# Optimization experiments

Measured on AMD Instinct MI355X. Metric: run time of the kernel, lower is better.

## Reference

```python
import jax, jax.numpy as jnp
import numpy as np

SHIFT_MAX = 20.0  # max |offset| in pixels; padded margin is (M-N)/2 = 32

def setup_inputs() -> dict:
    key = jax.random.key(0)
    k1, k2 = jax.random.split(key)
    B, M, N, C = 2048, 128, 64, 4
    padded_obj = jax.random.normal(k1, (B, M, M, 1), dtype=jnp.float32)
    # channel-format offsets (B,1,2,C): [...,0,:] = x (col) shift, [...,1,:] = y (row) shift
    positions = (jax.random.uniform(k2, (B, 1, 2, C), dtype=jnp.float32) - 0.5) * 2.0 * SHIFT_MAX
    return {"padded_obj": padded_obj, "positions": positions, "N": N}


def _bilinear_extract(padded_obj, positions, N):
    # padded_obj: (B,M,M,1), positions: (B,1,2,C) -> patches (B,N,N,C)
    # Equivalent to: translate each (per-channel) copy of the object by -offset
    # with bilinear interpolation and zero fill, then crop the central NxN.
    B, M = padded_obj.shape[0], padded_obj.shape[1]
    C = positions.shape[-1]
    img = padded_obj[..., 0]                       # (B,M,M)
    ox = positions[:, 0, 0, :]                     # (B,C) x (column) offset
    oy = positions[:, 0, 1, :]                     # (B,C) y (row) offset
    c0 = (M - N) // 2                              # crop origin
    r = jnp.arange(N, dtype=positions.dtype)
    # sample coordinates in source image: out(r,c) = img(r + c0 + oy, c + c0 + ox)
    yy = r[None, None, :] + c0 + oy[..., None]     # (B,C,N)
    xx = r[None, None, :] + c0 + ox[..., None]     # (B,C,N)
    y0 = jnp.floor(yy)
    x0 = jnp.floor(xx)
    wy = (yy - y0)[:, :, :, None]                  # (B,C,N,1) row frac
    wx = (xx - x0)[:, :, None, :]                  # (B,C,1,N) col frac
    y0i = y0.astype(jnp.int32)
    x0i = x0.astype(jnp.int32)
    b_idx = jnp.arange(B)[:, None, None, None]

    def gather(yi, xi):
        # yi: (B,C,N) rows, xi: (B,C,N) cols -> (B,C,N,N) with zero fill OOB
        valid = ((yi[:, :, :, None] >= 0) & (yi[:, :, :, None] < M)
                 & (xi[:, :, None, :] >= 0) & (xi[:, :, None, :] < M))
        yc = jnp.clip(yi, 0, M - 1)[:, :, :, None]
        xc = jnp.clip(xi, 0, M - 1)[:, :, None, :]
        vals = img[b_idx, yc, xc]                  # (B,C,N,N)
        return jnp.where(valid, vals, jnp.zeros((), vals.dtype))

    v00 = gather(y0i, x0i)
    v01 = gather(y0i, x0i + 1)
    v10 = gather(y0i + 1, x0i)
    v11 = gather(y0i + 1, x0i + 1)
    patch = (v00 * (1 - wy) * (1 - wx) + v01 * (1 - wy) * wx
             + v10 * wy * (1 - wx) + v11 * wy * wx)   # (B,C,N,N)
    return jnp.transpose(patch, (0, 2, 3, 1))          # (B,N,N,C)


def reference(padded_obj, positions, N):
    return _bilinear_extract(padded_obj, positions, N)
```

## Files before the change

kernel.cpp:

```cpp
#include <hip/hip_runtime.h>


constexpr int Mdim   = 128;
constexpr int Npatch = 64;
constexpr int Cc     = 4;
constexpr int C0     = 32;
constexpr int SROWS  = 74;

__global__ __launch_bounds__(512, 8) void extract_patches_kernel(
    const float* __restrict__ img,
    const float* __restrict__ pos,
    float* __restrict__ out)
{
    __shared__ float lds[SROWS * Mdim];

    const int bid  = blockIdx.x;
    const int b    = bid >> 1;
    const int h    = bid & 1;
    const float* __restrict__ imgb = img + (size_t)b * (Mdim * Mdim);
    const float* __restrict__ pb   = pos + (size_t)b * (2 * Cc);

    const int tid  = threadIdx.x;
    const int lane = tid & 63;
    const int wave = tid >> 6;

    float w00[Cc], w01[Cc], w10[Cc], w11[Cc];
    int   iyv[Cc], ixv[Cc];
#pragma unroll
    for (int c = 0; c < Cc; ++c) {
        const float ox = pb[c];
        const float oy = pb[Cc + c];
        const float fx = floorf(ox);
        const float fy = floorf(oy);
        const float wx = ox - fx;
        const float wy = oy - fy;
        ixv[c] = C0 + (int)fx;
        iyv[c] = C0 + (int)fy;
        w00[c] = (1.0f - wy) * (1.0f - wx);
        w01[c] = (1.0f - wy) * wx;
        w10[c] = wy * (1.0f - wx);
        w11[c] = wy * wx;
    }

    int min_iy = min(min(iyv[0], iyv[1]), min(iyv[2], iyv[3]));
    int r0 = min(min_iy + 32 * h, Mdim - SROWS);

    const float* src = imgb + r0 * Mdim;
    for (int w = wave; w < (SROWS * Mdim) / 256; w += 8) {
        const float* g = src + w * 256 + lane * 4;
        __builtin_amdgcn_global_load_lds(
            (const __attribute__((address_space(1))) void*)g,
            (__attribute__((address_space(3))) void*)&lds[w * 256],
            16, 0, 0);
    }

    __syncthreads();

    const int j   = tid & 63;
    const int s   = tid >> 6;
    const int li0 = s * 4;

    int   a[Cc];
    float p0[Cc], p1[Cc];
#pragma unroll
    for (int c = 0; c < Cc; ++c) {
        a[c] = (iyv[c] + 32 * h + li0 - r0) * Mdim + ixv[c] + j;
        p0[c] = lds[a[c]];
        p1[c] = lds[a[c] + 1];
    }

    float* obase = out + (((size_t)b * Npatch + 32 * h + li0) * Npatch + j) * Cc;
#pragma unroll
    for (int k = 0; k < 4; ++k) {
        float4 o;
        float* res = reinterpret_cast<float*>(&o);
#pragma unroll
        for (int c = 0; c < Cc; ++c) {
            a[c] += Mdim;
            const float n0 = lds[a[c]];
            const float n1 = lds[a[c] + 1];
            res[c] = w00[c] * p0[c] + w01[c] * p1[c] + w10[c] * n0 + w11[c] * n1;
            p0[c] = n0;
            p1[c] = n1;
        }
        *reinterpret_cast<float4*>(obase + (size_t)k * Npatch * Cc) = o;
    }
}

extern "C" void kernel_launch(void* const* d_in, const int* in_sizes, int n_in,
                              void* d_out, int out_size, void* d_ws, size_t ws_size,
                              hipStream_t stream) {
    const float* img = (const float*)d_in[0];
    const float* pos = (const float*)d_in[1];
    float* out = (float*)d_out;

    const int B = in_sizes[0] / (Mdim * Mdim);
    extract_patches_kernel<<<dim3(2 * B), dim3(512), 0, stream>>>(img, pos, out);
}
```

Baseline: 231.8 us.

## Make blocks persistent over eight work items with double-buffered LDS prefetch

Each block now processes eight (batch, half) items instead of one, and double-buffers the LDS staging so the global-to-LDS copy of the next item overlaps the interpolation of the current one, controlled by explicit vmcnt waits and barriers. The goal is to hide load latency and amortize block launch and setup costs. In exchange LDS per block doubles, occupancy drops to 4 blocks, and the grid shrinks to 512 blocks, which may underfill the GPU. The staging window grows to 76 rows so the 5 chunks per wave come out even.

After: 235.7 us. Within noise of the previous version (+1.7%).

```diff
diff --git a/kernel.cpp b/kernel.cpp
--- a/kernel.cpp
+++ b/kernel.cpp
@@ -5,85 +5,125 @@
 constexpr int Npatch = 64;
 constexpr int Cc     = 4;
 constexpr int C0     = 32;
-constexpr int SROWS  = 74;
+constexpr int SROWS  = 76;
+constexpr int CHUNKS = (SROWS * Mdim) / 256;
+constexpr int CPW    = 5;
+constexpr int ITEMS  = 8;
 
-__global__ __launch_bounds__(512, 8) void extract_patches_kernel(
+__global__ __launch_bounds__(512, 4) void extract_patches_kernel(
     const float* __restrict__ img,
     const float* __restrict__ pos,
     float* __restrict__ out)
 {
-    __shared__ float lds[SROWS * Mdim];
-
-    const int bid  = blockIdx.x;
-    const int b    = bid >> 1;
-    const int h    = bid & 1;
-    const float* __restrict__ imgb = img + (size_t)b * (Mdim * Mdim);
-    const float* __restrict__ pb   = pos + (size_t)b * (2 * Cc);
+    __shared__ float lds[2][SROWS * Mdim];
 
     const int tid  = threadIdx.x;
     const int lane = tid & 63;
     const int wave = tid >> 6;
 
-    float w00[Cc], w01[Cc], w10[Cc], w11[Cc];
-    int   iyv[Cc], ixv[Cc];
+    const int item0 = blockIdx.x * ITEMS;
+    const int b0    = item0 >> 1;
+
+    float oxv[4][Cc], oyv[4][Cc];
 #pragma unroll
-    for (int c = 0; c < Cc; ++c) {
-        const float ox = pb[c];
-        const float oy = pb[Cc + c];
-        const float fx = floorf(ox);
-        const float fy = floorf(oy);
-        const float wx = ox - fx;
-        const float wy = oy - fy;
-        ixv[c] = C0 + (int)fx;
-        iyv[c] = C0 + (int)fy;
-        w00[c] = (1.0f - wy) * (1.0f - wx);
-        w01[c] = (1.0f - wy) * wx;
-        w10[c] = wy * (1.0f - wx);
-        w11[c] = wy * wx;
+    for (int q = 0; q < 4; ++q) {
+        const float* pb = pos + (size_t)(b0 + q) * (2 * Cc);
+#pragma unroll
+        for (int c = 0; c < Cc; ++c) { oxv[q][c] = pb[c]; oyv[q][c] = pb[Cc + c]; }
     }
 
-    int min_iy = min(min(iyv[0], iyv[1]), min(iyv[2], iyv[3]));
-    int r0 = min(min_iy + 32 * h, Mdim - SROWS);
+    int   iyC[Cc], ixC[Cc], r0C; float wC[Cc][4];
+    int   iyN[Cc], ixN[Cc], r0N; float wN[Cc][4];
 
-    const float* src = imgb + r0 * Mdim;
-    for (int w = wave; w < (SROWS * Mdim) / 256; w += 8) {
-        const float* g = src + w * 256 + lane * 4;
-        __builtin_amdgcn_global_load_lds(
-            (const __attribute__((address_space(1))) void*)g,
-            (__attribute__((address_space(3))) void*)&lds[w * 256],
-            16, 0, 0);
-    }
-
-    __syncthreads();
-
-    const int j   = tid & 63;
-    const int s   = tid >> 6;
-    const int li0 = s * 4;
-
-    int   a[Cc];
-    float p0[Cc], p1[Cc];
-#pragma unroll
-    for (int c = 0; c < Cc; ++c) {
-        a[c] = (iyv[c] + 32 * h + li0 - r0) * Mdim + ixv[c] + j;
-        p0[c] = lds[a[c]];
-        p1[c] = lds[a[c] + 1];
-    }
-
-    float* obase = out + (((size_t)b * Npatch + 32 * h + li0) * Npatch + j) * Cc;
-#pragma unroll
-    for (int k = 0; k < 4; ++k) {
-        float4 o;
-        float* res = reinterpret_cast<float*>(&o);
+    auto make_consts = [&](int t, int* iy, int* ix, float (*w)[4], int& r0) {
+        const int q = (t >> 1) & 3, h = t & 1;
+        int mn = Mdim;
 #pragma unroll
         for (int c = 0; c < Cc; ++c) {
-            a[c] += Mdim;
-            const float n0 = lds[a[c]];
-            const float n1 = lds[a[c] + 1];
-            res[c] = w00[c] * p0[c] + w01[c] * p1[c] + w10[c] * n0 + w11[c] * n1;
-            p0[c] = n0;
-            p1[c] = n1;
+            const float ox = oxv[q][c], oy = oyv[q][c];
+            const float fx = floorf(ox), fy = floorf(oy);
+            const float wx = ox - fx,   wy = oy - fy;
+            ix[c] = C0 + (int)fx;
+            iy[c] = C0 + (int)fy;
+            w[c][0] = (1.f - wy) * (1.f - wx);
+            w[c][1] = (1.f - wy) * wx;
+            w[c][2] = wy * (1.f - wx);
+            w[c][3] = wy * wx;
+            mn = min(mn, iy[c]);
         }
-        *reinterpret_cast<float4*>(obase + (size_t)k * Npatch * Cc) = o;
+        r0 = min(mn + 32 * h, Mdim - SROWS);
+    };
+
+    auto stage = [&](int t, int r0) {
+        const int b = (item0 + t) >> 1;
+        const float* src = img + (size_t)b * (Mdim * Mdim) + r0 * Mdim;
+        float* dst = &lds[t & 1][0];
+#pragma unroll
+        for (int k = 0; k < CPW; ++k) {
+            const int wc = min(wave + 8 * k, CHUNKS - 1);
+            __builtin_amdgcn_global_load_lds(
+                (const __attribute__((address_space(1))) void*)(src + wc * 256 + lane * 4),
+                (__attribute__((address_space(3))) void*)(dst + wc * 256),
+                16, 0, 0);
+        }
+    };
+
+    auto compute = [&](int t, const int* iy, const int* ix, const float (*w)[4], int r0) {
+        const int b = (item0 + t) >> 1, h = t & 1;
+        const float* buf = &lds[t & 1][0];
+        const int li0 = wave * 4;
+        const int j   = lane;
+        int a[Cc]; float p0[Cc], p1[Cc];
+#pragma unroll
+        for (int c = 0; c < Cc; ++c) {
+            a[c]  = (iy[c] + 32 * h + li0 - r0) * Mdim + ix[c] + j;
+            p0[c] = buf[a[c]];
+            p1[c] = buf[a[c] + 1];
+        }
+        float* obase = out + (((size_t)b * Npatch + 32 * h + li0) * Npatch + j) * Cc;
+#pragma unroll
+        for (int k = 0; k < 4; ++k) {
+            float4 o; float* res = reinterpret_cast<float*>(&o);
+#pragma unroll
+            for (int c = 0; c < Cc; ++c) {
+                a[c] += Mdim;
+                const float n0 = buf[a[c]], n1 = buf[a[c] + 1];
+                res[c] = w[c][0] * p0[c] + w[c][1] * p1[c] + w[c][2] * n0 + w[c][3] * n1;
+                p0[c] = n0; p1[c] = n1;
+            }
+            *reinterpret_cast<float4*>(obase + (size_t)k * Npatch * Cc) = o;
+        }
+    };
+
+    make_consts(0, iyC, ixC, wC, r0C);
+    stage(0, r0C);
+
+#pragma unroll
+    for (int t = 0; t < ITEMS; ++t) {
+        if (t + 1 < ITEMS) {
+            make_consts(t + 1, iyN, ixN, wN, r0N);
+            stage(t + 1, r0N);
+            asm volatile("s_waitcnt vmcnt(5)" ::: "memory");
+        } else {
+            asm volatile("s_waitcnt vmcnt(0)" ::: "memory");
+        }
+        __builtin_amdgcn_s_barrier();
+        asm volatile("" ::: "memory");
+
+        compute(t, iyC, ixC, wC, r0C);
+
+        asm volatile("" ::: "memory");
+        __builtin_amdgcn_s_barrier();
+
+        if (t + 1 < ITEMS) {
+#pragma unroll
+            for (int c = 0; c < Cc; ++c) {
+                iyC[c] = iyN[c]; ixC[c] = ixN[c];
+#pragma unroll
+                for (int z = 0; z < 4; ++z) wC[c][z] = wN[c][z];
+            }
+            r0C = r0N;
+        }
     }
 }
 
@@ -95,5 +135,6 @@
     float* out = (float*)d_out;
 
     const int B = in_sizes[0] / (Mdim * Mdim);
-    extract_patches_kernel<<<dim3(2 * B), dim3(512), 0, stream>>>(img, pos, out);
+    const int nblocks = (2 * B) / ITEMS;
+    extract_patches_kernel<<<dim3(nblocks), dim3(512), 0, stream>>>(img, pos, out);
 }
```
